# Kernel optimization log

Hardware: AMD Instinct MI355X
Metric: run time of the kernel (lower is better)

Reference implementation:

```python
import jax, jax.numpy as jnp
import numpy as np

D_MODEL = 1024
NUM_HEADS = 16
ENERGY_SCALE = 0.1
LN_EPS = 1e-5


def layernorm(x, gamma, beta):
    mu = jnp.mean(x, axis=-1, keepdims=True)
    var = jnp.var(x, axis=-1, keepdims=True)
    return (x - mu) * jax.lax.rsqrt(var + LN_EPS) * gamma + beta


def setup_inputs() -> dict:
    key = jax.random.key(0)
    ks = jax.random.split(key, 8)
    B, L, D = 2, 2048, D_MODEL
    s = 0.02
    return {
        "x": jax.random.normal(ks[0], (B, L, D), dtype=jnp.float32),
        "wq": jax.random.normal(ks[1], (D, D), dtype=jnp.float32) * s,
        "wk": jax.random.normal(ks[2], (D, D), dtype=jnp.float32) * s,
        "wv": jax.random.normal(ks[3], (D, D), dtype=jnp.float32) * s,
        "wo_w": jax.random.normal(ks[4], (D, D), dtype=jnp.float32) * s,
        "wo_b": jnp.zeros((D,), dtype=jnp.float32),
        "ep_w": jax.random.normal(ks[5], (D, D), dtype=jnp.float32) * s,
        "ep_b": jnp.zeros((D,), dtype=jnp.float32),
        "en_g": jnp.ones((D,), dtype=jnp.float32),
        "en_b": jnp.zeros((D,), dtype=jnp.float32),
        "ln_g": jnp.ones((D,), dtype=jnp.float32),
        "ln_b": jnp.zeros((D,), dtype=jnp.float32),
    }


def reference(x, wq, wk, wv, wo_w, wo_b, ep_w, ep_b, en_g, en_b, ln_g, ln_b):
    B, L, D = x.shape
    H, dk = NUM_HEADS, D // NUM_HEADS
    # Linear projections (torch convention: y = x @ W^T), split heads -> [B,H,L,dk]
    q = (x @ wq.T).reshape(B, L, H, dk).transpose(0, 2, 1, 3)
    k = (x @ wk.T).reshape(B, L, H, dk).transpose(0, 2, 1, 3)
    v = (x @ wv.T).reshape(B, L, H, dk).transpose(0, 2, 1, 3)
    scores = jnp.einsum("bhld,bhmd->bhlm", q, k) / jnp.sqrt(jnp.float32(dk))
    # Energy bias: ef @ ef^T as a proper GEMM (same math as the broadcast-mul-sum)
    ef = layernorm(x @ ep_w.T + ep_b, en_g, en_b)
    energy_bias = jnp.einsum("bld,bmd->blm", ef, ef)  # [B,L,L]
    scores = scores + ENERGY_SCALE * energy_bias[:, None, :, :]
    attn = jax.nn.softmax(scores, axis=-1)  # dropout is identity in eval mode
    ctx = jnp.einsum("bhlm,bhmd->bhld", attn, v)
    ctx = ctx.transpose(0, 2, 1, 3).reshape(B, L, D)
    out = ctx @ wo_w.T + wo_b
    return layernorm(out + x, ln_g, ln_b), attn
```

## Files before the change

kernel.cpp:

```cpp
#include <hip/hip_runtime.h>
#include <math.h>

#define D_MODEL 1024
#define NUM_HEADS 16
#define DK 64
#define L_SEQ 2048
#define BATCH 2
#define LN_EPS 1e-5f
#define ENERGY_SCALE 0.1f

typedef __attribute__((ext_vector_type(8))) short short8;
typedef __attribute__((ext_vector_type(4))) float f32x4;
typedef __attribute__((address_space(1))) const unsigned int gas_u32;
typedef __attribute__((address_space(3))) unsigned int las_u32;

__device__ __forceinline__ float waveReduceSum(float v) {
#pragma unroll
    for (int off = 32; off > 0; off >>= 1) v += __shfl_xor(v, off, 64);
    return v;
}

__device__ __forceinline__ unsigned short f2bf(float f) {
    unsigned int u = __float_as_uint(f);
    u += 0x7fff + ((u >> 16) & 1);
    return (unsigned short)(u >> 16);
}
__device__ __forceinline__ float bf2f(unsigned short u) {
    return __uint_as_float((unsigned int)u << 16);
}

__global__ __launch_bounds__(256) void cvt6(
    const float* s0, const float* s1, const float* s2,
    const float* s3, const float* s4, const float* s5,
    unsigned short* d0, unsigned short* d1, unsigned short* d2,
    unsigned short* d3, unsigned short* d4, unsigned short* d5,
    long long n0, long long n1, long long n2, long long n3, long long n4, long long n5)
{
    const float* s; unsigned short* d; long long n;
    switch (blockIdx.y) {
        case 0: s = s0; d = d0; n = n0; break;
        case 1: s = s1; d = d1; n = n1; break;
        case 2: s = s2; d = d2; n = n2; break;
        case 3: s = s3; d = d3; n = n3; break;
        case 4: s = s4; d = d4; n = n4; break;
        default: s = s5; d = d5; n = n5; break;
    }
    long long i = ((long long)blockIdx.x * 256 + threadIdx.x) * 4;
    if (i >= n) return;
    float4 v = *(const float4*)(s + i);
    ushort4 o;
    o.x = f2bf(v.x); o.y = f2bf(v.y); o.z = f2bf(v.z); o.w = f2bf(v.w);
    *(ushort4*)(d + i) = o;
}

__global__ __launch_bounds__(256) void gemm_bf16(
    const unsigned short* __restrict__ A, const unsigned short* __restrict__ B,
    const float* __restrict__ bias, float* __restrict__ Cf, unsigned short* __restrict__ Ch,
    int N, int K, long long sA, long long sB, long long sC,
    float* __restrict__ ebtmax)
{
    A += (long long)blockIdx.z * sA;
    B += (long long)blockIdx.z * sB;
    __shared__ unsigned short As[128 * 64];
    __shared__ unsigned short Bs[128 * 64];
    const int tid = threadIdx.x;
    const int lane = tid & 63, w = tid >> 6;
    const int quad = lane >> 4, col = lane & 15;
    const int wm = w & 1, wn = w >> 1;
    const int row0 = blockIdx.y * 128, col0 = blockIdx.x * 128;

    const int lr = lane >> 3, lc = lane & 7;
    const int gcs = (lc ^ lr) * 8;

    f32x4 acc[4][4];
#pragma unroll
    for (int mt = 0; mt < 4; mt++)
#pragma unroll
        for (int nt = 0; nt < 4; nt++) acc[mt][nt] = (f32x4){0.f, 0.f, 0.f, 0.f};

    for (int k0 = 0; k0 < K; k0 += 64) {
        __syncthreads();
#pragma unroll
        for (int p = 0; p < 4; p++) {
            const int rb = w * 32 + p * 8;
            __builtin_amdgcn_global_load_lds(
                (gas_u32*)(A + (long long)(row0 + rb + lr) * K + k0 + gcs),
                (las_u32*)(As + rb * 64), 16, 0, 0);
            __builtin_amdgcn_global_load_lds(
                (gas_u32*)(B + (long long)(col0 + rb + lr) * K + k0 + gcs),
                (las_u32*)(Bs + rb * 64), 16, 0, 0);
        }
        __syncthreads();
#pragma unroll
        for (int kc = 0; kc < 2; kc++) {
            const int csw = ((quad + 4 * kc) ^ (col & 7)) * 8;
            short8 af[4], bfr[4];
#pragma unroll
            for (int mt = 0; mt < 4; mt++)
                af[mt] = *(const short8*)(As + (wm * 64 + mt * 16 + col) * 64 + csw);
#pragma unroll
            for (int nt = 0; nt < 4; nt++)
                bfr[nt] = *(const short8*)(Bs + (wn * 64 + nt * 16 + col) * 64 + csw);
#pragma unroll
            for (int mt = 0; mt < 4; mt++)
#pragma unroll
                for (int nt = 0; nt < 4; nt++)
                    acc[mt][nt] = __builtin_amdgcn_mfma_f32_16x16x32_bf16(af[mt], bfr[nt], acc[mt][nt], 0, 0, 0);
        }
    }

#pragma unroll
    for (int mt = 0; mt < 4; mt++)
#pragma unroll
        for (int nt = 0; nt < 4; nt++)
#pragma unroll
            for (int reg = 0; reg < 4; reg++) {
                long long row = row0 + wm * 64 + mt * 16 + quad * 4 + reg;
                int c = col0 + wn * 64 + nt * 16 + col;
                float v = acc[mt][nt][reg];
                if (bias) v += bias[c];
                if (Cf) Cf[blockIdx.z * sC + row * N + c] = v;
                else    Ch[blockIdx.z * sC + row * N + c] = f2bf(v);
            }

    if (ebtmax) {
        const int tcol = blockIdx.x * 2 + wn;
#pragma unroll
        for (int mt = 0; mt < 4; mt++) {
            float mx[4];
#pragma unroll
            for (int reg = 0; reg < 4; reg++) mx[reg] = acc[mt][0][reg];
#pragma unroll
            for (int nt = 1; nt < 4; nt++)
#pragma unroll
                for (int reg = 0; reg < 4; reg++)
                    mx[reg] = fmaxf(mx[reg], acc[mt][nt][reg]);
#pragma unroll
            for (int off = 8; off > 0; off >>= 1)
#pragma unroll
                for (int reg = 0; reg < 4; reg++)
                    mx[reg] = fmaxf(mx[reg], __shfl_xor(mx[reg], off, 64));
            if (col == 0) {
                long long rowg = (long long)blockIdx.z * L_SEQ + row0 + wm * 64 + mt * 16 + quad * 4;
#pragma unroll
                for (int reg = 0; reg < 4; reg++)
                    ebtmax[(rowg + reg) * 32 + tcol] = bf2f(f2bf(mx[reg]));
            }
        }
    }
}

__global__ __launch_bounds__(256) void proj_gemm(
    const unsigned short* __restrict__ Xh,
    const unsigned short* __restrict__ wqh, const unsigned short* __restrict__ wkh,
    const unsigned short* __restrict__ wvh, const unsigned short* __restrict__ eph,
    const float* __restrict__ ep_b,
    unsigned short* __restrict__ Qh, unsigned short* __restrict__ Kh,
    unsigned short* __restrict__ Vf, float* __restrict__ EP,
    float* __restrict__ qn, float* __restrict__ kn)
{
    const unsigned short* B;
    switch (blockIdx.z) {
        case 0: B = wqh; break;
        case 1: B = wkh; break;
        case 2: B = wvh; break;
        default: B = eph; break;
    }
    __shared__ unsigned short As[128 * 64];
    __shared__ unsigned short Bs[128 * 64];
    const int tid = threadIdx.x;
    const int lane = tid & 63, w = tid >> 6;
    const int quad = lane >> 4, col = lane & 15;
    const int wm = w & 1, wn = w >> 1;
    const int row0 = blockIdx.y * 128, col0 = blockIdx.x * 128;
    const int K = D_MODEL, N = D_MODEL;

    const int lr = lane >> 3, lc = lane & 7;
    const int gcs = (lc ^ lr) * 8;

    f32x4 acc[4][4];
#pragma unroll
    for (int mt = 0; mt < 4; mt++)
#pragma unroll
        for (int nt = 0; nt < 4; nt++) acc[mt][nt] = (f32x4){0.f, 0.f, 0.f, 0.f};

    for (int k0 = 0; k0 < K; k0 += 64) {
        __syncthreads();
#pragma unroll
        for (int p = 0; p < 4; p++) {
            const int rb = w * 32 + p * 8;
            __builtin_amdgcn_global_load_lds(
                (gas_u32*)(Xh + (long long)(row0 + rb + lr) * K + k0 + gcs),
                (las_u32*)(As + rb * 64), 16, 0, 0);
            __builtin_amdgcn_global_load_lds(
                (gas_u32*)(B + (long long)(col0 + rb + lr) * K + k0 + gcs),
                (las_u32*)(Bs + rb * 64), 16, 0, 0);
        }
        __syncthreads();
#pragma unroll
        for (int kc = 0; kc < 2; kc++) {
            const int csw = ((quad + 4 * kc) ^ (col & 7)) * 8;
            short8 af[4], bfr[4];
#pragma unroll
            for (int mt = 0; mt < 4; mt++)
                af[mt] = *(const short8*)(As + (wm * 64 + mt * 16 + col) * 64 + csw);
#pragma unroll
            for (int nt = 0; nt < 4; nt++)
                bfr[nt] = *(const short8*)(Bs + (wn * 64 + nt * 16 + col) * 64 + csw);
#pragma unroll
            for (int mt = 0; mt < 4; mt++)
#pragma unroll
                for (int nt = 0; nt < 4; nt++)
                    acc[mt][nt] = __builtin_amdgcn_mfma_f32_16x16x32_bf16(af[mt], bfr[nt], acc[mt][nt], 0, 0, 0);
        }
    }

    unsigned short* Hout = (blockIdx.z == 0) ? Qh : (blockIdx.z == 1) ? Kh : Vf;
#pragma unroll
    for (int mt = 0; mt < 4; mt++)
#pragma unroll
        for (int nt = 0; nt < 4; nt++)
#pragma unroll
            for (int reg = 0; reg < 4; reg++) {
                long long row = row0 + wm * 64 + mt * 16 + quad * 4 + reg;
                int c = col0 + wn * 64 + nt * 16 + col;
                float v = acc[mt][nt][reg];
                if (blockIdx.z == 3) EP[row * N + c] = v + ep_b[c];
                else                 Hout[row * N + c] = f2bf(v);
            }

    if (blockIdx.z <= 1) {
        float* dst = (blockIdx.z == 0) ? qn : kn;
        const int hh = blockIdx.x * 2 + wn;
#pragma unroll
        for (int mt = 0; mt < 4; mt++) {
            float s2[4];
#pragma unroll
            for (int reg = 0; reg < 4; reg++) s2[reg] = 0.f;
#pragma unroll
            for (int nt = 0; nt < 4; nt++)
#pragma unroll
                for (int reg = 0; reg < 4; reg++)
                    s2[reg] += acc[mt][nt][reg] * acc[mt][nt][reg];
#pragma unroll
            for (int off = 8; off > 0; off >>= 1)
#pragma unroll
                for (int reg = 0; reg < 4; reg++)
                    s2[reg] += __shfl_xor(s2[reg], off, 64);
            if (col == 0) {
                int row = row0 + wm * 64 + mt * 16 + quad * 4;
                int bb = row >> 11, l = row & (L_SEQ - 1);
                float4 o;
                o.x = sqrtf(s2[0]); o.y = sqrtf(s2[1]);
                o.z = sqrtf(s2[2]); o.w = sqrtf(s2[3]);
                *(float4*)(dst + ((long long)(bb * NUM_HEADS + hh)) * L_SEQ + l) = o;
            }
        }
    }
}

__global__ __launch_bounds__(256) void ln_rows(
    const float* __restrict__ in, const float* __restrict__ res,
    const float* __restrict__ g, const float* __restrict__ bta,
    float* __restrict__ outf, unsigned short* __restrict__ outh)
{
    const long long row = blockIdx.x;
    const float* ip = in + row * D_MODEL;
    const float* rp = res ? res + row * D_MODEL : nullptr;
    const int tid = threadIdx.x;
    float vals[4];
    float s = 0.f, ss = 0.f;
#pragma unroll
    for (int j = 0; j < 4; j++) {
        int idx = tid + j * 256;
        float v = ip[idx];
        if (rp) v += rp[idx];
        vals[j] = v; s += v; ss += v * v;
    }
    __shared__ float sred[4], ssred[4];
    s = waveReduceSum(s); ss = waveReduceSum(ss);
    int wave = tid >> 6, lane = tid & 63;
    if (lane == 0) { sred[wave] = s; ssred[wave] = ss; }
    __syncthreads();
    float ts = sred[0] + sred[1] + sred[2] + sred[3];
    float tss = ssred[0] + ssred[1] + ssred[2] + ssred[3];
    float mu = ts * (1.f / D_MODEL);
    float var = tss * (1.f / D_MODEL) - mu * mu;
    float rs = rsqrtf(var + LN_EPS);
#pragma unroll
    for (int j = 0; j < 4; j++) {
        int idx = tid + j * 256;
        float o = (vals[j] - mu) * rs * g[idx] + bta[idx];
        if (outf) __builtin_nontemporal_store(o, outf + row * D_MODEL + idx);
        else      outh[row * D_MODEL + idx] = f2bf(o);
    }
}

__global__ __launch_bounds__(256) void transpose_v(
    const unsigned short* __restrict__ V, unsigned short* __restrict__ Vt)
{
    const int m0 = blockIdx.x * 64, h = blockIdx.y, b = blockIdx.z;
    __shared__ unsigned int t[64][65];
    const int tid = threadIdx.x;
    {
        int r = tid >> 4, c4 = (tid & 15) * 4;
#pragma unroll
        for (int i = 0; i < 4; i++) {
            int row = r + i * 16;
            ushort4 v = *(const ushort4*)(V + ((long long)b * L_SEQ + m0 + row) * D_MODEL + h * DK + c4);
            t[row][c4] = v.x; t[row][c4 + 1] = v.y; t[row][c4 + 2] = v.z; t[row][c4 + 3] = v.w;
        }
    }
    __syncthreads();
    const int lane = tid & 63, wv = tid >> 6;
#pragma unroll
    for (int i = 0; i < 16; i++) {
        int d = wv * 16 + i;
        Vt[(((long long)(b * NUM_HEADS + h)) * DK + d) * L_SEQ + m0 + lane] = (unsigned short)t[lane][d];
    }
}

__global__ __launch_bounds__(256) void kstats2(
    const float* __restrict__ kn, float* __restrict__ kmax, float* __restrict__ ktmax)
{
    const long long bh = blockIdx.x;
    const float* p = kn + bh * L_SEQ;
    const int tid = threadIdx.x;
    float4 a = *(const float4*)(p + tid * 8);
    float4 c = *(const float4*)(p + tid * 8 + 4);
    float m = fmaxf(fmaxf(fmaxf(a.x, a.y), fmaxf(a.z, a.w)),
                    fmaxf(fmaxf(c.x, c.y), fmaxf(c.z, c.w)));
    m = fmaxf(m, __shfl_xor(m, 1, 64));
    m = fmaxf(m, __shfl_xor(m, 2, 64));
    m = fmaxf(m, __shfl_xor(m, 4, 64));
    if ((tid & 7) == 0) ktmax[bh * 32 + (tid >> 3)] = m;
    m = fmaxf(m, __shfl_xor(m, 8, 64));
    m = fmaxf(m, __shfl_xor(m, 16, 64));
    m = fmaxf(m, __shfl_xor(m, 32, 64));
    __shared__ float red[4];
    if ((tid & 63) == 0) red[tid >> 6] = m;
    __syncthreads();
    if (tid == 0)
        kmax[bh] = fmaxf(fmaxf(red[0], red[1]), fmaxf(red[2], red[3]));
}

__global__ __launch_bounds__(64) void skip_mask(
    const float* __restrict__ ebtmax, const float* __restrict__ qn,
    const float* __restrict__ kmax, const float* __restrict__ ktmax,
    unsigned int* __restrict__ skipm, float* __restrict__ ebmax)
{
    const int l0 = blockIdx.x * 64, h = blockIdx.y, b = blockIdx.z;
    const int tid = threadIdx.x;
    const int row = l0 + tid;
    const int bh = b * NUM_HEADS + h;
    const float* ebt = ebtmax + ((long long)b * L_SEQ + row) * 32;
    float ebr[32];
#pragma unroll
    for (int t = 0; t < 32; t++) ebr[t] = ebt[t];
    float mx = ebr[0];
#pragma unroll
    for (int t = 1; t < 32; t++) mx = fmaxf(mx, ebr[t]);
    if (blockIdx.y == 0) ebmax[(long long)b * L_SEQ + row] = mx;

    float q = qn[(long long)bh * L_SEQ + row];
    float Mh = ENERGY_SCALE * mx + q * kmax[bh] * 0.125f + 0.02f;
    const float* ktm = ktmax + bh * 32;
    unsigned int m = 0;
#pragma unroll
    for (int t = 0; t < 32; t++) {
        float ub = ENERGY_SCALE * ebr[t] + q * ktm[t] * 0.125f;
        unsigned long long bal = __ballot(ub < Mh - 45.0f);
        if (bal == ~0ull) m |= (1u << t);
    }
    if (tid == 0) skipm[bh * 32 + blockIdx.x] = m;
}

__global__ __launch_bounds__(256) void attn_mfma(
    const unsigned short* __restrict__ Qh, const unsigned short* __restrict__ Kh,
    const unsigned short* __restrict__ Vt, const unsigned short* __restrict__ EBh,
    const float* __restrict__ ebmax, const float* __restrict__ qn,
    const float* __restrict__ kmax, const unsigned int* __restrict__ skipm,
    float* __restrict__ attn_out, unsigned short* __restrict__ CTXh)
{
    __shared__ unsigned short Ks[2][64 * 64];
    __shared__ unsigned short Vts[64 * 64];
    __shared__ unsigned short Ps[4 * 16 * 72];

    const int tid = threadIdx.x;
    const int lane = tid & 63, w = tid >> 6;
    const int quad = lane >> 4, col = lane & 15;
    const int l0 = blockIdx.x * 64;
    const int h = blockIdx.y, b = blockIdx.z;

    const unsigned int sm = skipm[(b * NUM_HEADS + h) * 32 + blockIdx.x];

    const unsigned short* kbase = Kh + ((long long)b * L_SEQ) * D_MODEL + h * DK;
    const unsigned short* vbase = Vt + ((long long)(b * NUM_HEADS + h)) * DK * L_SEQ;

    const int lr = lane >> 3, lc = lane & 7;
    const int gsw = (lc ^ lr) * 8;

    auto nxt = [&](int t) -> int {
        unsigned int rem = ~sm;
        if (t >= 0) rem &= (t >= 31) ? 0u : (0xFFFFFFFFu << (t + 1));
        return rem ? (int)__builtin_ctz(rem) : -1;
    };
    const int t0 = nxt(-1);

    if (t0 >= 0) {
#pragma unroll
        for (int p = 0; p < 2; p++) {
            const int rb = w * 8 + p * 32;
            __builtin_amdgcn_global_load_lds(
                (gas_u32*)(kbase + (long long)(t0 * 64 + rb + lr) * D_MODEL + gsw),
                (las_u32*)(&Ks[0][rb * 64]), 16, 0, 0);
        }
    }

    {
        float* zbase = attn_out + (((long long)(b * NUM_HEADS + h)) * L_SEQ + l0) * L_SEQ;
        const int zc = (tid & 15) * 4;
        const int zr = tid >> 4;
        const f32x4 zv = {0.f, 0.f, 0.f, 0.f};
        for (int t = 0; t < 32; t++) {
            if (!(sm & (1u << t))) continue;
            float* tb = zbase + t * 64 + zc;
#pragma unroll
            for (int rr = 0; rr < 4; rr++)
                __builtin_nontemporal_store(zv, (f32x4*)(tb + (long long)(rr * 16 + zr) * L_SEQ));
        }
    }

    short8 aq[2];
    {
        const unsigned short* qrow = Qh + ((long long)b * L_SEQ + l0 + w * 16 + col) * D_MODEL + h * DK;
        aq[0] = *(const short8*)(qrow + quad * 8);
        aq[1] = *(const short8*)(qrow + 32 + quad * 8);
    }

    float Mhat[4];
    {
        const float km = kmax[b * NUM_HEADS + h];
#pragma unroll
        for (int reg = 0; reg < 4; reg++) {
            int row = l0 + w * 16 + quad * 4 + reg;
            float qb = qn[((long long)(b * NUM_HEADS + h)) * L_SEQ + row];
            Mhat[reg] = ENERGY_SCALE * ebmax[(long long)b * L_SEQ + row] +
                        qb * km * 0.125f + 0.02f;
        }
    }

    const unsigned short* ebp = EBh + ((long long)b * L_SEQ + l0 + w * 16 + quad * 4) * L_SEQ + col;

    __syncthreads();

    float rowSacc[4] = {0.f, 0.f, 0.f, 0.f};
    int cur = 0;
    for (int t = t0; t >= 0; ) {
        const int tn = nxt(t);
        if (tn >= 0) {
#pragma unroll
            for (int p = 0; p < 2; p++) {
                const int rb = w * 8 + p * 32;
                __builtin_amdgcn_global_load_lds(
                    (gas_u32*)(kbase + (long long)(tn * 64 + rb + lr) * D_MODEL + gsw),
                    (las_u32*)(&Ks[cur ^ 1][rb * 64]), 16, 0, 0);
            }
        }
        const int m0 = t * 64;

        f32x4 acc[4];
#pragma unroll
        for (int nt = 0; nt < 4; nt++) acc[nt] = (f32x4){0.f, 0.f, 0.f, 0.f};
        __builtin_amdgcn_s_setprio(1);
#pragma unroll
        for (int nt = 0; nt < 4; nt++)
#pragma unroll
            for (int kc = 0; kc < 2; kc++) {
                short8 bk = *(const short8*)(&Ks[cur][((nt * 16 + col) << 6) +
                                                     (((quad + 4 * kc) ^ (col & 7)) << 3)]);
                acc[nt] = __builtin_amdgcn_mfma_f32_16x16x32_bf16(aq[kc], bk, acc[nt], 0, 0, 0);
            }
        __builtin_amdgcn_s_setprio(0);
#pragma unroll
        for (int nt = 0; nt < 4; nt++)
#pragma unroll
            for (int reg = 0; reg < 4; reg++) {
                float e = bf2f(ebp[(long long)reg * L_SEQ + m0 + nt * 16]);
                float s = acc[nt][reg] * 0.125f + ENERGY_SCALE * e;
                rowSacc[reg] += __expf(s - Mhat[reg]);
            }
        __syncthreads();
        cur ^= 1;
        t = tn;
    }

    float invS[4];
#pragma unroll
    for (int reg = 0; reg < 4; reg++) {
        float v = rowSacc[reg];
#pragma unroll
        for (int off = 8; off > 0; off >>= 1) v += __shfl_xor(v, off, 64);
        invS[reg] = 1.f / v;
    }

    cur = 0;
    if (t0 >= 0) {
#pragma unroll
        for (int p = 0; p < 2; p++) {
            const int rb = w * 8 + p * 32;
            __builtin_amdgcn_global_load_lds(
                (gas_u32*)(kbase + (long long)(t0 * 64 + rb + lr) * D_MODEL + gsw),
                (las_u32*)(&Ks[0][rb * 64]), 16, 0, 0);
        }
    }
    __syncthreads();

    f32x4 ctx[4];
#pragma unroll
    for (int nt = 0; nt < 4; nt++) ctx[nt] = (f32x4){0.f, 0.f, 0.f, 0.f};

    unsigned short* Psw = Ps + w * 16 * 72;
    float* aob = attn_out + (((long long)(b * NUM_HEADS + h)) * L_SEQ + l0 + w * 16 + quad * 4) * L_SEQ + col;

    for (int t = t0; t >= 0; ) {
        const int tn = nxt(t);
        const int m0 = t * 64;

#pragma unroll
        for (int p = 0; p < 2; p++) {
            const int rb = w * 8 + p * 32;
            __builtin_amdgcn_global_load_lds(
                (gas_u32*)(vbase + (long long)(rb + lr) * L_SEQ + m0 + gsw),
                (las_u32*)(&Vts[rb * 64]), 16, 0, 0);
        }
        if (tn >= 0) {
#pragma unroll
            for (int p = 0; p < 2; p++) {
                const int rb = w * 8 + p * 32;
                __builtin_amdgcn_global_load_lds(
                    (gas_u32*)(kbase + (long long)(tn * 64 + rb + lr) * D_MODEL + gsw),
                    (las_u32*)(&Ks[cur ^ 1][rb * 64]), 16, 0, 0);
            }
        }

        f32x4 acc[4];
#pragma unroll
        for (int nt = 0; nt < 4; nt++) acc[nt] = (f32x4){0.f, 0.f, 0.f, 0.f};
        __builtin_amdgcn_s_setprio(1);
#pragma unroll
        for (int nt = 0; nt < 4; nt++)
#pragma unroll
            for (int kc = 0; kc < 2; kc++) {
                short8 bk = *(const short8*)(&Ks[cur][((nt * 16 + col) << 6) +
                                                     (((quad + 4 * kc) ^ (col & 7)) << 3)]);
                acc[nt] = __builtin_amdgcn_mfma_f32_16x16x32_bf16(aq[kc], bk, acc[nt], 0, 0, 0);
            }
        __builtin_amdgcn_s_setprio(0);

#pragma unroll
        for (int nt = 0; nt < 4; nt++)
#pragma unroll
            for (int reg = 0; reg < 4; reg++) {
                float e = bf2f(ebp[(long long)reg * L_SEQ + m0 + nt * 16]);
                float s = acc[nt][reg] * 0.125f + ENERGY_SCALE * e;
                float p = __expf(s - Mhat[reg]) * invS[reg];
                acc[nt][reg] = p;
                Psw[(quad * 4 + reg) * 72 + nt * 16 + col] = f2bf(p);
            }
        __syncthreads();

#pragma unroll
        for (int nt = 0; nt < 4; nt++)
#pragma unroll
            for (int reg = 0; reg < 4; reg++)
                __builtin_nontemporal_store(acc[nt][reg],
                    aob + (long long)reg * L_SEQ + m0 + nt * 16);

        short8 ap[2];
#pragma unroll
        for (int kc = 0; kc < 2; kc++)
            ap[kc] = *(const short8*)(Psw + col * 72 + quad * 8 + kc * 32);
        __builtin_amdgcn_s_setprio(1);
#pragma unroll
        for (int nt = 0; nt < 4; nt++)
#pragma unroll
            for (int kc = 0; kc < 2; kc++) {
                short8 bv = *(const short8*)(&Vts[((nt * 16 + col) << 6) +
                                                  (((quad + 4 * kc) ^ (col & 7)) << 3)]);
                ctx[nt] = __builtin_amdgcn_mfma_f32_16x16x32_bf16(ap[kc], bv, ctx[nt], 0, 0, 0);
            }
        __builtin_amdgcn_s_setprio(0);
        __syncthreads();
        cur ^= 1;
        t = tn;
    }

#pragma unroll
    for (int nt = 0; nt < 4; nt++)
#pragma unroll
        for (int reg = 0; reg < 4; reg++)
            CTXh[((long long)b * L_SEQ + l0 + w * 16 + quad * 4 + reg) * D_MODEL + h * DK + nt * 16 + col] =
                f2bf(ctx[nt][reg]);
}

extern "C" void kernel_launch(void* const* d_in, const int* in_sizes, int n_in,
                              void* d_out, int out_size, void* d_ws, size_t ws_size,
                              hipStream_t stream) {
    const float* x    = (const float*)d_in[0];
    const float* wq   = (const float*)d_in[1];
    const float* wk   = (const float*)d_in[2];
    const float* wv   = (const float*)d_in[3];
    const float* wo_w = (const float*)d_in[4];
    const float* wo_b = (const float*)d_in[5];
    const float* ep_w = (const float*)d_in[6];
    const float* ep_b = (const float*)d_in[7];
    const float* en_g = (const float*)d_in[8];
    const float* en_b = (const float*)d_in[9];
    const float* ln_g = (const float*)d_in[10];
    const float* ln_b = (const float*)d_in[11];

    float* out_final = (float*)d_out;
    float* attn_out  = out_final + (long long)BATCH * L_SEQ * D_MODEL;

    const long long MD = (long long)BATCH * L_SEQ * D_MODEL;
    const long long WN = (long long)D_MODEL * D_MODEL;
    const long long BH = (long long)BATCH * NUM_HEADS;
    const long long LL = (long long)BATCH * L_SEQ * L_SEQ;

    unsigned short* EBh = (unsigned short*)d_ws;
    float* EP = (float*)(EBh + LL);
    unsigned short* Xh   = (unsigned short*)(EP + MD);
    unsigned short* Qh   = Xh + MD;
    unsigned short* Kh   = Qh + MD;
    unsigned short* Vf   = Kh + MD;
    unsigned short* Vt   = Vf + MD;
    unsigned short* EFh  = Vt + MD;
    unsigned short* CTXh = EFh + MD;
    unsigned short* wqh  = CTXh + MD;
    unsigned short* wkh  = wqh + WN;
    unsigned short* wvh  = wkh + WN;
    unsigned short* eph  = wvh + WN;
    unsigned short* woh  = eph + WN;
    float* ebmax  = (float*)(woh + WN);
    float* qn     = ebmax + (long long)BATCH * L_SEQ;
    float* kn     = qn + BH * L_SEQ;
    float* kmax   = kn + BH * L_SEQ;
    float* ktmax  = kmax + BH;
    float* ebtmax = ktmax + BH * 32;
    unsigned int* skipm = (unsigned int*)(ebtmax + (long long)BATCH * L_SEQ * 32);
    float* OUT = EP;

    const int M = BATCH * L_SEQ;
    dim3 blk(256);

    cvt6<<<dim3((unsigned)(MD / 1024), 6), blk, 0, stream>>>(
        x, wq, wk, wv, ep_w, wo_w, Xh, wqh, wkh, wvh, eph, woh,
        MD, WN, WN, WN, WN, WN);

    proj_gemm<<<dim3(D_MODEL / 128, M / 128, 4), blk, 0, stream>>>(
        Xh, wqh, wkh, wvh, eph, ep_b, Qh, Kh, Vf, EP, qn, kn);

    ln_rows<<<dim3(M), blk, 0, stream>>>(EP, nullptr, en_g, en_b, nullptr, EFh);

    gemm_bf16<<<dim3(L_SEQ / 128, L_SEQ / 128, BATCH), blk, 0, stream>>>(
        EFh, EFh, nullptr, nullptr, EBh, L_SEQ, D_MODEL,
        (long long)L_SEQ * D_MODEL, (long long)L_SEQ * D_MODEL,
        (long long)L_SEQ * L_SEQ, ebtmax);

    kstats2<<<dim3((unsigned)BH), blk, 0, stream>>>(kn, kmax, ktmax);
    skip_mask<<<dim3(L_SEQ / 64, NUM_HEADS, BATCH), dim3(64), 0, stream>>>(
        ebtmax, qn, kmax, ktmax, skipm, ebmax);

    transpose_v<<<dim3(L_SEQ / 64, NUM_HEADS, BATCH), blk, 0, stream>>>(Vf, Vt);

    attn_mfma<<<dim3(L_SEQ / 64, NUM_HEADS, BATCH), blk, 0, stream>>>(
        Qh, Kh, Vt, EBh, ebmax, qn, kmax, skipm, attn_out, CTXh);

    gemm_bf16<<<dim3(D_MODEL / 128, M / 128, 1), blk, 0, stream>>>(
        CTXh, woh, wo_b, OUT, nullptr, D_MODEL, D_MODEL, 0, 0, 0, nullptr);

    ln_rows<<<dim3(M), blk, 0, stream>>>(OUT, x, ln_g, ln_b, out_final, nullptr);
}
```

Measured before the change: 743.0 us.

## Fuse V transpose into projection GEMM epilogue and fold key stats into skip_mask

The V projection blocks now write their tile transposed through shared memory straight into the head-major Vt layout, which removes the separate transpose_v kernel and its extra global round trip. The kstats2 kernel is dropped and its per-tile and global key-norm maxima are recomputed inside skip_mask with wave shuffles, saving another launch. ln_rows is also vectorised to float4 loads and stores. The trade-offs are an extra shared-memory staging pass in the GEMM epilogue and some redundant key-norm reads in every skip_mask block.

```diff
diff --git a/kernel.cpp b/kernel.cpp
--- a/kernel.cpp
+++ b/kernel.cpp
@@ -156,7 +156,7 @@
     const unsigned short* __restrict__ wvh, const unsigned short* __restrict__ eph,
     const float* __restrict__ ep_b,
     unsigned short* __restrict__ Qh, unsigned short* __restrict__ Kh,
-    unsigned short* __restrict__ Vf, float* __restrict__ EP,
+    unsigned short* __restrict__ Vt, float* __restrict__ EP,
     float* __restrict__ qn, float* __restrict__ kn)
 {
     const unsigned short* B;
@@ -215,7 +215,42 @@
         }
     }
 
-    unsigned short* Hout = (blockIdx.z == 0) ? Qh : (blockIdx.z == 1) ? Kh : Vf;
+    if (blockIdx.z == 2) {
+        const int b = row0 >> 11;
+        const int l0loc = row0 & (L_SEQ - 1);
+#pragma unroll
+        for (int ch = 0; ch < 2; ch++)
+#pragma unroll
+            for (int rh = 0; rh < 2; rh++) {
+                __syncthreads();
+                if (wm == rh && wn == ch) {
+#pragma unroll
+                    for (int mt = 0; mt < 4; mt++)
+#pragma unroll
+                        for (int nt = 0; nt < 4; nt++)
+#pragma unroll
+                            for (int reg = 0; reg < 4; reg++) {
+                                int r = mt * 16 + quad * 4 + reg;
+                                int c = nt * 16 + col;
+                                Bs[c * 64 + (r ^ ((c & 7) << 3))] = f2bf(acc[mt][nt][reg]);
+                            }
+                }
+                __syncthreads();
+                const int hh = blockIdx.x * 2 + ch;
+#pragma unroll
+                for (int it = 0; it < 2; it++) {
+                    int dd = it * 32 + (tid >> 3);
+                    int lcn = (tid & 7) * 8;
+                    short8 v = *(const short8*)(Bs + dd * 64 + (lcn ^ ((dd & 7) << 3)));
+                    long long dst = (((long long)(b * NUM_HEADS + hh)) * DK + dd) * L_SEQ
+                                    + l0loc + rh * 64 + lcn;
+                    *(short8*)(Vt + dst) = v;
+                }
+            }
+        return;
+    }
+
+    unsigned short* Hout = (blockIdx.z == 0) ? Qh : Kh;
 #pragma unroll
     for (int mt = 0; mt < 4; mt++)
 #pragma unroll
@@ -268,15 +303,14 @@
     const float* ip = in + row * D_MODEL;
     const float* rp = res ? res + row * D_MODEL : nullptr;
     const int tid = threadIdx.x;
-    float vals[4];
-    float s = 0.f, ss = 0.f;
-#pragma unroll
-    for (int j = 0; j < 4; j++) {
-        int idx = tid + j * 256;
-        float v = ip[idx];
-        if (rp) v += rp[idx];
-        vals[j] = v; s += v; ss += v * v;
-    }
+    const int idx = tid * 4;
+    float4 v = *(const float4*)(ip + idx);
+    if (rp) {
+        float4 r = *(const float4*)(rp + idx);
+        v.x += r.x; v.y += r.y; v.z += r.z; v.w += r.w;
+    }
+    float s = v.x + v.y + v.z + v.w;
+    float ss = v.x * v.x + v.y * v.y + v.z * v.z + v.w * v.w;
     __shared__ float sred[4], ssred[4];
     s = waveReduceSum(s); ss = waveReduceSum(ss);
     int wave = tid >> 6, lane = tid & 63;
@@ -287,72 +321,54 @@
     float mu = ts * (1.f / D_MODEL);
     float var = tss * (1.f / D_MODEL) - mu * mu;
     float rs = rsqrtf(var + LN_EPS);
-#pragma unroll
-    for (int j = 0; j < 4; j++) {
-        int idx = tid + j * 256;
-        float o = (vals[j] - mu) * rs * g[idx] + bta[idx];
-        if (outf) __builtin_nontemporal_store(o, outf + row * D_MODEL + idx);
-        else      outh[row * D_MODEL + idx] = f2bf(o);
-    }
-}
-
-__global__ __launch_bounds__(256) void transpose_v(
-    const unsigned short* __restrict__ V, unsigned short* __restrict__ Vt)
-{
-    const int m0 = blockIdx.x * 64, h = blockIdx.y, b = blockIdx.z;
-    __shared__ unsigned int t[64][65];
-    const int tid = threadIdx.x;
-    {
-        int r = tid >> 4, c4 = (tid & 15) * 4;
-#pragma unroll
-        for (int i = 0; i < 4; i++) {
-            int row = r + i * 16;
-            ushort4 v = *(const ushort4*)(V + ((long long)b * L_SEQ + m0 + row) * D_MODEL + h * DK + c4);
-            t[row][c4] = v.x; t[row][c4 + 1] = v.y; t[row][c4 + 2] = v.z; t[row][c4 + 3] = v.w;
-        }
-    }
-    __syncthreads();
-    const int lane = tid & 63, wv = tid >> 6;
-#pragma unroll
-    for (int i = 0; i < 16; i++) {
-        int d = wv * 16 + i;
-        Vt[(((long long)(b * NUM_HEADS + h)) * DK + d) * L_SEQ + m0 + lane] = (unsigned short)t[lane][d];
-    }
-}
-
-__global__ __launch_bounds__(256) void kstats2(
-    const float* __restrict__ kn, float* __restrict__ kmax, float* __restrict__ ktmax)
-{
-    const long long bh = blockIdx.x;
-    const float* p = kn + bh * L_SEQ;
-    const int tid = threadIdx.x;
-    float4 a = *(const float4*)(p + tid * 8);
-    float4 c = *(const float4*)(p + tid * 8 + 4);
-    float m = fmaxf(fmaxf(fmaxf(a.x, a.y), fmaxf(a.z, a.w)),
-                    fmaxf(fmaxf(c.x, c.y), fmaxf(c.z, c.w)));
-    m = fmaxf(m, __shfl_xor(m, 1, 64));
-    m = fmaxf(m, __shfl_xor(m, 2, 64));
-    m = fmaxf(m, __shfl_xor(m, 4, 64));
-    if ((tid & 7) == 0) ktmax[bh * 32 + (tid >> 3)] = m;
-    m = fmaxf(m, __shfl_xor(m, 8, 64));
-    m = fmaxf(m, __shfl_xor(m, 16, 64));
-    m = fmaxf(m, __shfl_xor(m, 32, 64));
-    __shared__ float red[4];
-    if ((tid & 63) == 0) red[tid >> 6] = m;
-    __syncthreads();
-    if (tid == 0)
-        kmax[bh] = fmaxf(fmaxf(red[0], red[1]), fmaxf(red[2], red[3]));
+    float4 gg = *(const float4*)(g + idx);
+    float4 bb = *(const float4*)(bta + idx);
+    if (outf) {
+        f32x4 o;
+        o[0] = (v.x - mu) * rs * gg.x + bb.x;
+        o[1] = (v.y - mu) * rs * gg.y + bb.y;
+        o[2] = (v.z - mu) * rs * gg.z + bb.z;
+        o[3] = (v.w - mu) * rs * gg.w + bb.w;
+        __builtin_nontemporal_store(o, (f32x4*)(outf + row * D_MODEL + idx));
+    } else {
+        ushort4 o;
+        o.x = f2bf((v.x - mu) * rs * gg.x + bb.x);
+        o.y = f2bf((v.y - mu) * rs * gg.y + bb.y);
+        o.z = f2bf((v.z - mu) * rs * gg.z + bb.z);
+        o.w = f2bf((v.w - mu) * rs * gg.w + bb.w);
+        *(ushort4*)(outh + row * D_MODEL + idx) = o;
+    }
 }
 
 __global__ __launch_bounds__(64) void skip_mask(
     const float* __restrict__ ebtmax, const float* __restrict__ qn,
-    const float* __restrict__ kmax, const float* __restrict__ ktmax,
-    unsigned int* __restrict__ skipm, float* __restrict__ ebmax)
+    const float* __restrict__ kn,
+    unsigned int* __restrict__ skipm, float* __restrict__ ebmax,
+    float* __restrict__ kmaxg)
 {
     const int l0 = blockIdx.x * 64, h = blockIdx.y, b = blockIdx.z;
     const int tid = threadIdx.x;
     const int row = l0 + tid;
     const int bh = b * NUM_HEADS + h;
+
+    float ktm_pair;
+    {
+        const float* p = kn + (long long)bh * L_SEQ + (tid >> 1) * 64 + (tid & 1) * 32;
+        float4 a = *(const float4*)(p);
+        float m = fmaxf(fmaxf(a.x, a.y), fmaxf(a.z, a.w));
+#pragma unroll
+        for (int i = 4; i < 32; i += 4) {
+            float4 c = *(const float4*)(p + i);
+            m = fmaxf(m, fmaxf(fmaxf(c.x, c.y), fmaxf(c.z, c.w)));
+        }
+        m = fmaxf(m, __shfl_xor(m, 1, 64));
+        ktm_pair = m;
+    }
+    float km = ktm_pair;
+#pragma unroll
+    for (int off = 2; off < 64; off <<= 1) km = fmaxf(km, __shfl_xor(km, off, 64));
+    if (blockIdx.x == 0 && tid == 0) kmaxg[bh] = km;
+
     const float* ebt = ebtmax + ((long long)b * L_SEQ + row) * 32;
     float ebr[32];
 #pragma unroll
@@ -363,12 +379,12 @@
     if (blockIdx.y == 0) ebmax[(long long)b * L_SEQ + row] = mx;
 
     float q = qn[(long long)bh * L_SEQ + row];
-    float Mh = ENERGY_SCALE * mx + q * kmax[bh] * 0.125f + 0.02f;
-    const float* ktm = ktmax + bh * 32;
+    float Mh = ENERGY_SCALE * mx + q * km * 0.125f + 0.02f;
     unsigned int m = 0;
 #pragma unroll
     for (int t = 0; t < 32; t++) {
-        float ub = ENERGY_SCALE * ebr[t] + q * ktm[t] * 0.125f;
+        float kt = __shfl(ktm_pair, 2 * t, 64);
+        float ub = ENERGY_SCALE * ebr[t] + q * kt * 0.125f;
         unsigned long long bal = __ballot(ub < Mh - 45.0f);
         if (bal == ~0ull) m |= (1u << t);
     }
@@ -633,8 +649,8 @@
     unsigned short* Xh   = (unsigned short*)(EP + MD);
     unsigned short* Qh   = Xh + MD;
     unsigned short* Kh   = Qh + MD;
-    unsigned short* Vf   = Kh + MD;
-    unsigned short* Vt   = Vf + MD;
+    unsigned short* Vfu  = Kh + MD;
+    unsigned short* Vt   = Vfu + MD;
     unsigned short* EFh  = Vt + MD;
     unsigned short* CTXh = EFh + MD;
     unsigned short* wqh  = CTXh + MD;
@@ -646,8 +662,8 @@
     float* qn     = ebmax + (long long)BATCH * L_SEQ;
     float* kn     = qn + BH * L_SEQ;
     float* kmax   = kn + BH * L_SEQ;
-    float* ktmax  = kmax + BH;
-    float* ebtmax = ktmax + BH * 32;
+    float* ktmaxu = kmax + BH;
+    float* ebtmax = ktmaxu + BH * 32;
     unsigned int* skipm = (unsigned int*)(ebtmax + (long long)BATCH * L_SEQ * 32);
     float* OUT = EP;
 
@@ -659,7 +675,7 @@
         MD, WN, WN, WN, WN, WN);
 
     proj_gemm<<<dim3(D_MODEL / 128, M / 128, 4), blk, 0, stream>>>(
-        Xh, wqh, wkh, wvh, eph, ep_b, Qh, Kh, Vf, EP, qn, kn);
+        Xh, wqh, wkh, wvh, eph, ep_b, Qh, Kh, Vt, EP, qn, kn);
 
     ln_rows<<<dim3(M), blk, 0, stream>>>(EP, nullptr, en_g, en_b, nullptr, EFh);
 
@@ -668,11 +684,8 @@
         (long long)L_SEQ * D_MODEL, (long long)L_SEQ * D_MODEL,
         (long long)L_SEQ * L_SEQ, ebtmax);
 
-    kstats2<<<dim3((unsigned)BH), blk, 0, stream>>>(kn, kmax, ktmax);
     skip_mask<<<dim3(L_SEQ / 64, NUM_HEADS, BATCH), dim3(64), 0, stream>>>(
-        ebtmax, qn, kmax, ktmax, skipm, ebmax);
-
-    transpose_v<<<dim3(L_SEQ / 64, NUM_HEADS, BATCH), blk, 0, stream>>>(Vf, Vt);
+        ebtmax, qn, kn, skipm, ebmax, kmax);
 
     attn_mfma<<<dim3(L_SEQ / 64, NUM_HEADS, BATCH), blk, 0, stream>>>(
         Qh, Kh, Vt, EBh, ebmax, qn, kmax, skipm, attn_out, CTXh);
```

New measurement: 735.3 us. No clear change (-1.0%).
